# Kernel tuning notes

Measured on AMD Instinct MI355X. Metric: run time of the kernel, lower is better.

Reference implementation:

```python
import jax, jax.numpy as jnp
import numpy as np

EMPHASIS_FACTOR = 1.5
TOP_K_PERCENT = 0.2


def setup_inputs() -> dict:
    key = jax.random.key(0)
    k1, k2 = jax.random.split(key)
    B, S, D = 32, 8192, 256
    x = jax.random.normal(k1, (B, S, D), dtype=jnp.float32)
    W = jax.random.normal(k2, (D, 1), dtype=jnp.float32) * (1.0 / np.sqrt(D))
    b = jnp.zeros((1,), dtype=jnp.float32)
    return {"x": x, "W": W, "b": b}


def reference(x, W, b):
    B, S, D = x.shape
    # e = tanh(x @ W + b): [B, S, 1]
    e = jnp.tanh(jnp.einsum('bsd,do->bso', x, W) + b)
    # softmax over seq axis, squeeze -> [B, S]
    a = jax.nn.softmax(e, axis=1)[..., 0]
    # top-k selection: k = max(1, int(S * top_k_percent)), static under jit
    k = max(1, int(S * TOP_K_PERCENT))
    _, top_k_idx = jax.lax.top_k(a, k)  # [B, k]
    # mask of top-k positions (equiv to one_hot + reduce_max, but a direct scatter)
    mask = jnp.zeros((B, S), dtype=bool).at[jnp.arange(B)[:, None], top_k_idx].set(True)
    emphasized_a = jnp.where(mask, a * EMPHASIS_FACTOR, a)  # [B, S]
    # weighted sum over seq -> [B, D]
    summed_output = jnp.einsum('bsd,bs->bd', x, emphasized_a)
    return summed_output, emphasized_a
```

## Files before the change

kernel.cpp:

```cpp
#include <hip/hip_runtime.h>
#include <math.h>

#define BB 32
#define SS 8192
#define DD 256
#define K_SEL 1638
#define EMPH 1.5f
#define HBINS 2048
#define HCH 8
#define IDX_STRIDE 1664
#define K5_BLOCKS 8
#define K5_SLICE 205
#define NCHUNK 64
#define ROWS_PER_BLOCK (SS / NCHUNK)

__device__ __forceinline__ unsigned monokey(float f) {
    unsigned u = __float_as_uint(f);
    return u ^ ((u & 0x80000000u) ? 0xFFFFFFFFu : 0x80000000u);
}

__global__ __launch_bounds__(1024) void k1_e_hist_s1(const float* __restrict__ x,
                                                     const float* __restrict__ W,
                                                     const float* __restrict__ bias,
                                                     float* __restrict__ e_ws,
                                                     unsigned* __restrict__ hist_ws,
                                                     float* __restrict__ s1part,
                                                     float* __restrict__ zpart) {
    __shared__ unsigned hist[HBINS];
    __shared__ float red[16 * 256];
    __shared__ float zred;
    const int tid = threadIdx.x;
    const int lane = tid & 63;
    const int wv = tid >> 6;
    for (int i = tid; i < HBINS; i += 1024) hist[i] = 0;
    if (tid == 0) zred = 0.0f;

    const int b = blockIdx.x >> 3;
    const int ch = blockIdx.x & 7;
    const int row0 = ch * 1024;

    const float4* W4 = (const float4*)W;
    const int cg = lane & 15;
    const float4 w0 = W4[cg];
    const float4 w1 = W4[cg + 16];
    const float4 w2 = W4[cg + 32];
    const float4 w3 = W4[cg + 48];
    const float bias0 = bias[0];
    __syncthreads();

    const float* xb = x + (size_t)b * SS * DD;
    float* eb = e_ws + (size_t)b * SS;

    float acc[16];
    #pragma unroll
    for (int m = 0; m < 16; m++) acc[m] = 0.0f;
    float zloc = 0.0f;

    for (int it = 0; it < 16; it++) {
        const int r = row0 + (it * 16 + wv) * 4 + (lane >> 4);
        const float4* rp = (const float4*)(xb + (size_t)r * DD);
        float4 a0 = rp[cg];
        float4 a1 = rp[cg + 16];
        float4 a2 = rp[cg + 32];
        float4 a3 = rp[cg + 48];
        float p = a0.x * w0.x + a0.y * w0.y + a0.z * w0.z + a0.w * w0.w;
        p += a1.x * w1.x + a1.y * w1.y + a1.z * w1.z + a1.w * w1.w;
        p += a2.x * w2.x + a2.y * w2.y + a2.z * w2.z + a2.w * w2.w;
        p += a3.x * w3.x + a3.y * w3.y + a3.z * w3.z + a3.w * w3.w;
        p += __shfl_xor(p, 1, 64);
        p += __shfl_xor(p, 2, 64);
        p += __shfl_xor(p, 4, 64);
        p += __shfl_xor(p, 8, 64);
        float ev = tanhf(p + bias0);
        float w = expf(ev);
        if (cg == 0) {
            eb[r] = ev;
            atomicAdd(&hist[monokey(ev) >> 21], 1u);
            zloc += w;
        }
        acc[0] += w * a0.x;  acc[1] += w * a0.y;  acc[2] += w * a0.z;  acc[3] += w * a0.w;
        acc[4] += w * a1.x;  acc[5] += w * a1.y;  acc[6] += w * a1.z;  acc[7] += w * a1.w;
        acc[8] += w * a2.x;  acc[9] += w * a2.y;  acc[10] += w * a2.z; acc[11] += w * a2.w;
        acc[12] += w * a3.x; acc[13] += w * a3.y; acc[14] += w * a3.z; acc[15] += w * a3.w;
    }
    #pragma unroll
    for (int m = 0; m < 16; m++) {
        acc[m] += __shfl_xor(acc[m], 16, 64);
        acc[m] += __shfl_xor(acc[m], 32, 64);
    }
    zloc += __shfl_xor(zloc, 16, 64);
    zloc += __shfl_xor(zloc, 32, 64);
    if (lane == 0) atomicAdd(&zred, zloc);
    if (lane < 16) {
        #pragma unroll
        for (int m = 0; m < 16; m++) red[wv * 256 + lane * 16 + m] = acc[m];
    }
    __syncthreads();
    unsigned* hout = hist_ws + (size_t)blockIdx.x * HBINS;
    for (int i = tid; i < HBINS; i += 1024) hout[i] = hist[i];
    if (tid == 0) zpart[blockIdx.x] = zred;
    if (tid < 256) {
        const int d = tid;
        const int q = d >> 6;
        const int cg2 = (d >> 2) & 15;
        const int j = d & 3;
        const int m = q * 4 + j;
        float s = 0.0f;
        #pragma unroll
        for (int w = 0; w < 16; w++) s += red[w * 256 + cg2 * 16 + m];
        s1part[(size_t)blockIdx.x * DD + d] = s;
    }
}

__global__ __launch_bounds__(1024) void k2_select(const float* __restrict__ e_ws,
                                                  const unsigned* __restrict__ hist_ws,
                                                  const float* __restrict__ zpart,
                                                  float* __restrict__ ea_out,
                                                  float* __restrict__ zinv,
                                                  int* __restrict__ idx_ws) {
    const int b = blockIdx.x;
    const int tid = threadIdx.x;
    const int lane = tid & 63;
    const int wid = tid >> 6;

    __shared__ float se[SS];
    __shared__ unsigned binTot[HBINS];
    __shared__ unsigned gsuf[257];
    __shared__ unsigned hsuf[129];
    __shared__ unsigned h7[128];
    __shared__ unsigned ecnt[128];
    __shared__ unsigned ebase[128];
    __shared__ unsigned uvar[2];
    __shared__ unsigned selCnt;
    __shared__ float fvar;

    const float* eg = e_ws + (size_t)b * SS;
    float* og = ea_out + (size_t)b * SS;
    int* il = idx_ws + (size_t)b * IDX_STRIDE;

    #pragma unroll
    for (int i = 0; i < 8; i++) {
        int s = tid + i * 1024;
        se[s] = eg[s];
    }
    if (tid == 0) {
        float z = 0.0f;
        #pragma unroll
        for (int c = 0; c < HCH; c++) z += zpart[b * HCH + c];
        fvar = 1.0f / z;
        zinv[b] = fvar;
        selCnt = 0;
    }
    unsigned c0 = 0, c1 = 0;
    for (int ch = 0; ch < HCH; ch++) {
        const unsigned* hc = hist_ws + ((size_t)(b * HCH + ch)) * HBINS;
        c0 += hc[2 * tid];
        c1 += hc[2 * tid + 1];
    }
    binTot[2 * tid] = c0;
    binTot[2 * tid + 1] = c1;
    __syncthreads();

    if (wid == 0) {
        unsigned g[4];
        unsigned tot = 0;
        #pragma unroll
        for (int j = 0; j < 4; j++) {
            unsigned s = 0;
            #pragma unroll
            for (int m = 0; m < 8; m++) s += binTot[(lane * 4 + j) * 8 + m];
            g[j] = s;
            tot += s;
        }
        unsigned xx = tot;
        #pragma unroll
        for (int off = 1; off < 64; off <<= 1) {
            unsigned v = __shfl_down(xx, off, 64);
            if (lane + off < 64) xx += v;
        }
        unsigned Snext = __shfl_down(xx, 1, 64);
        if (lane == 63) Snext = 0;
        unsigned s3 = Snext + g[3];
        unsigned s2 = s3 + g[2];
        unsigned s1 = s2 + g[1];
        unsigned s0 = s1 + g[0];
        gsuf[4 * lane] = s0; gsuf[4 * lane + 1] = s1;
        gsuf[4 * lane + 2] = s2; gsuf[4 * lane + 3] = s3;
        if (lane == 63) gsuf[256] = 0;
    }
    __syncthreads();

    if (tid < 256) {
        unsigned above = gsuf[tid + 1];
        if (above < K_SEL && K_SEL <= gsuf[tid]) {
            unsigned running = above;
            for (int j = 7; j >= 0; j--) {
                unsigned c = binTot[tid * 8 + j];
                if (running < K_SEL && K_SEL <= running + c) {
                    uvar[0] = (unsigned)(tid * 8 + j);
                    uvar[1] = K_SEL - running;
                    break;
                }
                running += c;
            }
        }
    }
    __syncthreads();
    unsigned prefix = uvar[0];
    unsigned kk = uvar[1];

    #pragma unroll
    for (int pass = 0; pass < 3; pass++) {
        const int shift = 14 - 7 * pass;
        if (tid < 128) h7[tid] = 0;
        __syncthreads();
        #pragma unroll
        for (int i = 0; i < 8; i++) {
            unsigned key = monokey(se[tid + i * 1024]);
            if ((key >> (shift + 7)) == prefix)
                atomicAdd(&h7[(key >> shift) & 127u], 1u);
        }
        __syncthreads();
        if (wid == 0) {
            unsigned a0 = h7[2 * lane];
            unsigned a1 = h7[2 * lane + 1];
            unsigned tot = a0 + a1;
            unsigned xx = tot;
            #pragma unroll
            for (int off = 1; off < 64; off <<= 1) {
                unsigned v = __shfl_down(xx, off, 64);
                if (lane + off < 64) xx += v;
            }
            unsigned Snext = __shfl_down(xx, 1, 64);
            if (lane == 63) Snext = 0;
            unsigned t1 = Snext + a1;
            unsigned t0 = t1 + a0;
            hsuf[2 * lane] = t0;
            hsuf[2 * lane + 1] = t1;
            if (lane == 63) hsuf[128] = 0;
        }
        __syncthreads();
        if (tid < 128) {
            unsigned above = hsuf[tid + 1];
            if (above < kk && kk <= hsuf[tid]) {
                uvar[0] = (prefix << 7) | (unsigned)tid;
                uvar[1] = kk - above;
            }
        }
        __syncthreads();
        prefix = uvar[0];
        kk = uvar[1];
    }
    const unsigned T = prefix;
    const unsigned r = kk;
    const float invZ = fvar;

    #pragma unroll
    for (int c = 0; c < 8; c++) {
        int s = c * 1024 + tid;
        unsigned long long bal = __ballot(monokey(se[s]) == T);
        if (lane == 0) ecnt[c * 16 + wid] = (unsigned)__popcll(bal);
    }
    __syncthreads();
    if (wid == 0) {
        unsigned a0 = ecnt[2 * lane];
        unsigned a1 = ecnt[2 * lane + 1];
        unsigned tot = a0 + a1;
        unsigned xx = tot;
        #pragma unroll
        for (int off = 1; off < 64; off <<= 1) {
            unsigned v = __shfl_up(xx, off, 64);
            if (lane >= off) xx += v;
        }
        ebase[2 * lane] = xx - tot;
        ebase[2 * lane + 1] = xx - a1;
    }
    __syncthreads();
    #pragma unroll
    for (int c = 0; c < 8; c++) {
        int s = c * 1024 + tid;
        float v = se[s];
        unsigned key = monokey(v);
        bool eq = (key == T);
        bool gt = (key > T);
        unsigned long long bal = __ballot(eq);
        unsigned myPref = (unsigned)__popcll(bal & ((1ull << lane) - 1ull));
        unsigned rank = ebase[c * 16 + wid] + myPref;
        bool sel = gt || (eq && rank < r);
        float a = expf(v) * invZ;
        og[s] = sel ? a * EMPH : a;
        if (sel) {
            unsigned slot = atomicAdd(&selCnt, 1u);
            il[slot] = s;
        }
    }
}

__global__ __launch_bounds__(256) void k5_corr(const float* __restrict__ x,
                                               const float* __restrict__ ea,
                                               const int* __restrict__ idx_ws,
                                               float* __restrict__ corr) {
    const int b = blockIdx.x >> 3;
    const int j = blockIdx.x & 7;
    const int lane = threadIdx.x & 63;
    const int wid = threadIdx.x >> 6;
    const int lo = j * K5_SLICE;
    const int hi = (lo + K5_SLICE < K_SEL) ? lo + K5_SLICE : K_SEL;
    const int* il = idx_ws + (size_t)b * IDX_STRIDE;
    const float* xb = x + (size_t)b * SS * DD;
    const float* ab = ea + (size_t)b * SS;
    float4 acc = make_float4(0.f, 0.f, 0.f, 0.f);
    for (int t = lo + wid; t < hi; t += 4) {
        int s = il[t];
        float w = ab[s] * (1.0f / 3.0f);
        float4 x4 = ((const float4*)(xb + (size_t)s * DD))[lane];
        acc.x += w * x4.x; acc.y += w * x4.y; acc.z += w * x4.z; acc.w += w * x4.w;
    }
    __shared__ float lds[4 * 256];
    ((float4*)lds)[wid * 64 + lane] = acc;
    __syncthreads();
    const int t = threadIdx.x;
    float v = lds[t] + lds[256 + t] + lds[512 + t] + lds[768 + t];
    corr[(size_t)blockIdx.x * DD + t] = v;
}

__global__ __launch_bounds__(256) void k6_final(const float* __restrict__ s1part,
                                                const float* __restrict__ corr,
                                                const float* __restrict__ zinv,
                                                float* __restrict__ out) {
    const int b = blockIdx.x;
    const int d = threadIdx.x;
    float s1 = 0.0f;
    #pragma unroll
    for (int ch = 0; ch < HCH; ch++) s1 += s1part[((size_t)b * HCH + ch) * DD + d];
    float c = 0.0f;
    #pragma unroll
    for (int j = 0; j < K5_BLOCKS; j++) c += corr[((size_t)b * K5_BLOCKS + j) * DD + d];
    out[b * DD + d] = s1 * zinv[b] + c;
}

__global__ __launch_bounds__(256) void f1_dot_tanh(const float* __restrict__ x,
                                                   const float* __restrict__ W,
                                                   const float* __restrict__ bias,
                                                   float* __restrict__ e) {
    const int lane = threadIdx.x & 63;
    const int wib  = threadIdx.x >> 6;
    const int waveId = blockIdx.x * 4 + wib;
    const int totalWaves = gridDim.x * 4;
    const float4 w4 = ((const float4*)W)[lane];
    const float bias0 = bias[0];
    for (int row = waveId; row < BB * SS; row += totalWaves) {
        float4 x4 = ((const float4*)(x + (size_t)row * DD))[lane];
        float p = x4.x * w4.x + x4.y * w4.y + x4.z * w4.z + x4.w * w4.w;
        #pragma unroll
        for (int off = 32; off >= 1; off >>= 1)
            p += __shfl_xor(p, off, 64);
        if (lane == 0) e[row] = tanhf(p + bias0);
    }
}
__global__ __launch_bounds__(1024) void f2_softmax_topk(float* __restrict__ ea) {
    const int b = blockIdx.x;
    const int tid = threadIdx.x;
    const int lane = tid & 63;
    const int wid  = tid >> 6;
    __shared__ float se[SS];
    __shared__ float wredf[16];
    __shared__ unsigned hist[256];
    __shared__ unsigned ssum[256];
    __shared__ unsigned wcnt[16];
    __shared__ unsigned uvar[3];
    __shared__ float fvar[1];
    float* eg = ea + (size_t)b * SS;
    float lsum = 0.0f;
    #pragma unroll
    for (int i = 0; i < 8; i++) {
        int s = tid + i * 1024;
        float v = eg[s];
        se[s] = v;
        lsum += expf(v);
    }
    #pragma unroll
    for (int off = 32; off >= 1; off >>= 1)
        lsum += __shfl_xor(lsum, off, 64);
    if (lane == 0) wredf[wid] = lsum;
    __syncthreads();
    if (tid == 0) {
        float z = 0.0f;
        for (int w = 0; w < 16; w++) z += wredf[w];
        fvar[0] = 1.0f / z;
    }
    __syncthreads();
    const float invZ = fvar[0];
    unsigned kk = K_SEL;
    unsigned prefix = 0;
    for (int byte = 3; byte >= 0; byte--) {
        if (tid < 256) hist[tid] = 0;
        __syncthreads();
        #pragma unroll
        for (int i = 0; i < 8; i++) {
            unsigned key = monokey(se[tid + i * 1024]);
            bool active = (byte == 3) || ((key >> ((byte + 1) * 8)) == prefix);
            if (active) atomicAdd(&hist[(key >> (byte * 8)) & 0xFFu], 1u);
        }
        __syncthreads();
        if (tid < 256) ssum[tid] = hist[tid];
        __syncthreads();
        for (int off = 1; off < 256; off <<= 1) {
            unsigned add = 0;
            if (tid < 256 && tid + off < 256) add = ssum[tid + off];
            __syncthreads();
            if (tid < 256) ssum[tid] += add;
            __syncthreads();
        }
        if (tid < 256) {
            unsigned above = (tid == 255) ? 0u : ssum[tid + 1];
            if (above < kk && kk <= ssum[tid]) {
                uvar[0] = (unsigned)tid;
                uvar[1] = kk - above;
            }
        }
        __syncthreads();
        prefix = (prefix << 8) | uvar[0];
        kk = uvar[1];
        __syncthreads();
    }
    const unsigned T = prefix;
    const unsigned r = kk;
    if (tid == 0) uvar[2] = 0;
    __syncthreads();
    for (int chunk = 0; chunk < 8; chunk++) {
        int s = chunk * 1024 + tid;
        float v = se[s];
        unsigned key = monokey(v);
        bool gt = key > T;
        bool eq = (key == T);
        unsigned long long bal = __ballot(eq);
        unsigned waveTot = (unsigned)__popcll(bal);
        unsigned myPref = (unsigned)__popcll(bal & ((1ull << lane) - 1ull));
        if (lane == 0) wcnt[wid] = waveTot;
        __syncthreads();
        unsigned base = uvar[2];
        for (int w = 0; w < wid; w++) base += wcnt[w];
        bool sel = gt || (eq && (base + myPref) < r);
        float a = expf(v) * invZ;
        eg[s] = sel ? a * EMPH : a;
        __syncthreads();
        if (tid == 0) {
            unsigned t = uvar[2];
            for (int w = 0; w < 16; w++) t += wcnt[w];
            uvar[2] = t;
        }
        __syncthreads();
    }
}
__global__ __launch_bounds__(256) void f0_zero(float* __restrict__ p, int n) {
    int i = blockIdx.x * blockDim.x + threadIdx.x;
    if (i < n) p[i] = 0.0f;
}
__global__ __launch_bounds__(256) void f3_weighted_atomic(const float* __restrict__ x,
                                                          const float* __restrict__ ea,
                                                          float* __restrict__ out) {
    const int blk = blockIdx.x;
    const int b = blk / NCHUNK;
    const int chunk = blk % NCHUNK;
    const int lane = threadIdx.x & 63;
    const int wid  = threadIdx.x >> 6;
    const float* xb = x + ((size_t)b * SS + (size_t)chunk * ROWS_PER_BLOCK) * DD;
    const float* ab = ea + (size_t)b * SS + (size_t)chunk * ROWS_PER_BLOCK;
    float4 acc = make_float4(0.f, 0.f, 0.f, 0.f);
    for (int rr = wid; rr < ROWS_PER_BLOCK; rr += 4) {
        float4 x4 = ((const float4*)(xb + (size_t)rr * DD))[lane];
        float a = ab[rr];
        acc.x += x4.x * a; acc.y += x4.y * a; acc.z += x4.z * a; acc.w += x4.w * a;
    }
    __shared__ float lds[4 * 256];
    ((float4*)lds)[wid * 64 + lane] = acc;
    __syncthreads();
    const int t = threadIdx.x;
    float v = lds[t] + lds[256 + t] + lds[512 + t] + lds[768 + t];
    atomicAdd(&out[b * 256 + t], v);
}

extern "C" void kernel_launch(void* const* d_in, const int* in_sizes, int n_in,
                              void* d_out, int out_size, void* d_ws, size_t ws_size,
                              hipStream_t stream) {
    (void)in_sizes; (void)n_in; (void)out_size;
    const float* x    = (const float*)d_in[0];
    const float* W    = (const float*)d_in[1];
    const float* bias = (const float*)d_in[2];
    float* out = (float*)d_out;
    float* sum_out = out;
    float* ea = out + BB * DD;

    const size_t e_bytes    = (size_t)BB * SS * sizeof(float);
    const size_t hist_bytes = (size_t)BB * HCH * HBINS * sizeof(unsigned);
    const size_t s1_bytes   = (size_t)BB * HCH * DD * sizeof(float);
    const size_t corr_bytes = (size_t)BB * K5_BLOCKS * DD * sizeof(float);
    const size_t zinv_bytes = 128;
    const size_t zpart_bytes= (size_t)BB * HCH * sizeof(float);
    const size_t idx_bytes  = (size_t)BB * IDX_STRIDE * sizeof(int);
    const size_t need = e_bytes + hist_bytes + s1_bytes + corr_bytes + zinv_bytes
                      + zpart_bytes + idx_bytes;

    if (ws_size >= need) {
        char* p = (char*)d_ws;
        float*    e_ws    = (float*)p;                 p += e_bytes;
        unsigned* hist_ws = (unsigned*)p;              p += hist_bytes;
        float*    s1part  = (float*)p;                 p += s1_bytes;
        float*    corr    = (float*)p;                 p += corr_bytes;
        float*    zinv    = (float*)p;                 p += zinv_bytes;
        float*    zpart   = (float*)p;                 p += zpart_bytes;
        int*      idx_ws  = (int*)p;

        k1_e_hist_s1<<<BB * HCH, 1024, 0, stream>>>(x, W, bias, e_ws, hist_ws, s1part, zpart);
        k2_select<<<BB, 1024, 0, stream>>>(e_ws, hist_ws, zpart, ea, zinv, idx_ws);
        k5_corr<<<BB * K5_BLOCKS, 256, 0, stream>>>(x, ea, idx_ws, corr);
        k6_final<<<BB, 256, 0, stream>>>(s1part, corr, zinv, sum_out);
    } else {
        f1_dot_tanh<<<4096, 256, 0, stream>>>(x, W, bias, ea);
        f2_softmax_topk<<<BB, 1024, 0, stream>>>(ea);
        f0_zero<<<(BB * DD + 255) / 256, 256, 0, stream>>>(sum_out, BB * DD);
        f3_weighted_atomic<<<BB * NCHUNK, 256, 0, stream>>>(x, ea, sum_out);
    }
}
```

Measured before the change: 397.8 us.

## Split selection so output write and top-k correction run across 16 chunks per batch

The per-batch select kernel now only finds the threshold key and a per-chunk tie quota. A new kernel with 16 blocks per batch then writes the emphasized attention, gathers the selected indices into shared memory, and accumulates the correction sum directly, which removes the global index list and the 32-block serial write phase. The cost is per-iteration block syncs for the tie-rank bookkeeping and twice as many correction partials to reduce at the end.

```diff
diff --git a/kernel.cpp b/kernel.cpp
--- a/kernel.cpp
+++ b/kernel.cpp
@@ -8,9 +8,8 @@
 #define EMPH 1.5f
 #define HBINS 2048
 #define HCH 8
-#define IDX_STRIDE 1664
-#define K5_BLOCKS 8
-#define K5_SLICE 205
+#define NCH3 16
+#define CH3_ROWS (SS / NCH3)
 #define NCHUNK 64
 #define ROWS_PER_BLOCK (SS / NCHUNK)
 
@@ -112,12 +111,11 @@
     }
 }
 
-__global__ __launch_bounds__(1024) void k2_select(const float* __restrict__ e_ws,
+__global__ __launch_bounds__(1024) void k2_thresh(const float* __restrict__ e_ws,
                                                   const unsigned* __restrict__ hist_ws,
                                                   const float* __restrict__ zpart,
-                                                  float* __restrict__ ea_out,
                                                   float* __restrict__ zinv,
-                                                  int* __restrict__ idx_ws) {
+                                                  unsigned* __restrict__ tq_ws) {
     const int b = blockIdx.x;
     const int tid = threadIdx.x;
     const int lane = tid & 63;
@@ -128,15 +126,10 @@
     __shared__ unsigned gsuf[257];
     __shared__ unsigned hsuf[129];
     __shared__ unsigned h7[128];
-    __shared__ unsigned ecnt[128];
-    __shared__ unsigned ebase[128];
+    __shared__ unsigned tie16[NCH3];
     __shared__ unsigned uvar[2];
-    __shared__ unsigned selCnt;
-    __shared__ float fvar;
 
     const float* eg = e_ws + (size_t)b * SS;
-    float* og = ea_out + (size_t)b * SS;
-    int* il = idx_ws + (size_t)b * IDX_STRIDE;
 
     #pragma unroll
     for (int i = 0; i < 8; i++) {
@@ -147,9 +140,7 @@
         float z = 0.0f;
         #pragma unroll
         for (int c = 0; c < HCH; c++) z += zpart[b * HCH + c];
-        fvar = 1.0f / z;
-        zinv[b] = fvar;
-        selCnt = 0;
+        zinv[b] = 1.0f / z;
     }
     unsigned c0 = 0, c1 = 0;
     for (int ch = 0; ch < HCH; ch++) {
@@ -253,75 +244,112 @@
     }
     const unsigned T = prefix;
     const unsigned r = kk;
-    const float invZ = fvar;
-
-    #pragma unroll
-    for (int c = 0; c < 8; c++) {
-        int s = c * 1024 + tid;
-        unsigned long long bal = __ballot(monokey(se[s]) == T);
-        if (lane == 0) ecnt[c * 16 + wid] = (unsigned)__popcll(bal);
-    }
-    __syncthreads();
-    if (wid == 0) {
-        unsigned a0 = ecnt[2 * lane];
-        unsigned a1 = ecnt[2 * lane + 1];
-        unsigned tot = a0 + a1;
-        unsigned xx = tot;
-        #pragma unroll
-        for (int off = 1; off < 64; off <<= 1) {
-            unsigned v = __shfl_up(xx, off, 64);
-            if (lane >= off) xx += v;
-        }
-        ebase[2 * lane] = xx - tot;
-        ebase[2 * lane + 1] = xx - a1;
-    }
-    __syncthreads();
-    #pragma unroll
-    for (int c = 0; c < 8; c++) {
-        int s = c * 1024 + tid;
-        float v = se[s];
+
+    if (tid < NCH3) tie16[tid] = 0;
+    __syncthreads();
+    #pragma unroll
+    for (int i = 0; i < 8; i++) {
+        int s = i * 1024 + tid;
+        unsigned long long beq = __ballot(monokey(se[s]) == T);
+        if (lane == 0) atomicAdd(&tie16[s >> 9], (unsigned)__popcll(beq));
+    }
+    __syncthreads();
+    if (tid == 0) {
+        unsigned run = 0;
+        unsigned* tq = tq_ws + b * 32;
+        tq[0] = T;
+        for (int c = 0; c < NCH3; c++) {
+            unsigned tc = tie16[c];
+            unsigned q = (r > run) ? (r - run) : 0u;
+            if (q > tc) q = tc;
+            tq[1 + c] = q;
+            run += tc;
+        }
+    }
+}
+
+__global__ __launch_bounds__(256) void k3_write_corr(const float* __restrict__ x,
+                                                     const float* __restrict__ e_ws,
+                                                     const unsigned* __restrict__ tq_ws,
+                                                     const float* __restrict__ zinv,
+                                                     float* __restrict__ ea_out,
+                                                     float* __restrict__ corr) {
+    const int b = blockIdx.x >> 4;
+    const int ch = blockIdx.x & 15;
+    const int tid = threadIdx.x;
+    const int lane = tid & 63;
+    const int wid = tid >> 6;
+
+    const unsigned* tq = tq_ws + b * 32;
+    const unsigned T = tq[0];
+    const unsigned quota = tq[1 + ch];
+    const float invZ = zinv[b];
+    const int s0 = ch * CH3_ROWS;
+    const float* eg = e_ws + (size_t)b * SS;
+    float* og = ea_out + (size_t)b * SS;
+
+    __shared__ int lidx[CH3_ROWS];
+    __shared__ float lw[CH3_ROWS];
+    __shared__ float lds[4 * 256];
+    __shared__ unsigned wtie[4];
+    __shared__ unsigned tieRun;
+    __shared__ unsigned selCnt;
+    if (tid == 0) { tieRun = 0; selCnt = 0; }
+    __syncthreads();
+
+    #pragma unroll
+    for (int i = 0; i < CH3_ROWS / 256; i++) {
+        int s = s0 + i * 256 + tid;
+        float v = eg[s];
         unsigned key = monokey(v);
+        bool gt = key > T;
         bool eq = (key == T);
-        bool gt = (key > T);
-        unsigned long long bal = __ballot(eq);
-        unsigned myPref = (unsigned)__popcll(bal & ((1ull << lane) - 1ull));
-        unsigned rank = ebase[c * 16 + wid] + myPref;
-        bool sel = gt || (eq && rank < r);
+        unsigned long long beq = __ballot(eq);
+        if (lane == 0) wtie[wid] = (unsigned)__popcll(beq);
+        __syncthreads();
+        unsigned base = tieRun;
+        for (int w = 0; w < wid; w++) base += wtie[w];
+        unsigned rank = base + (unsigned)__popcll(beq & ((1ull << lane) - 1ull));
+        bool sel = gt || (eq && rank < quota);
         float a = expf(v) * invZ;
         og[s] = sel ? a * EMPH : a;
         if (sel) {
             unsigned slot = atomicAdd(&selCnt, 1u);
-            il[slot] = s;
-        }
-    }
-}
-
-__global__ __launch_bounds__(256) void k5_corr(const float* __restrict__ x,
-                                               const float* __restrict__ ea,
-                                               const int* __restrict__ idx_ws,
-                                               float* __restrict__ corr) {
-    const int b = blockIdx.x >> 3;
-    const int j = blockIdx.x & 7;
-    const int lane = threadIdx.x & 63;
-    const int wid = threadIdx.x >> 6;
-    const int lo = j * K5_SLICE;
-    const int hi = (lo + K5_SLICE < K_SEL) ? lo + K5_SLICE : K_SEL;
-    const int* il = idx_ws + (size_t)b * IDX_STRIDE;
+            lidx[slot] = s;
+            lw[slot] = 0.5f * a;
+        }
+        __syncthreads();
+        if (tid == 0) tieRun += wtie[0] + wtie[1] + wtie[2] + wtie[3];
+        __syncthreads();
+    }
+
     const float* xb = x + (size_t)b * SS * DD;
-    const float* ab = ea + (size_t)b * SS;
-    float4 acc = make_float4(0.f, 0.f, 0.f, 0.f);
-    for (int t = lo + wid; t < hi; t += 4) {
-        int s = il[t];
-        float w = ab[s] * (1.0f / 3.0f);
-        float4 x4 = ((const float4*)(xb + (size_t)s * DD))[lane];
-        acc.x += w * x4.x; acc.y += w * x4.y; acc.z += w * x4.z; acc.w += w * x4.w;
-    }
-    __shared__ float lds[4 * 256];
-    ((float4*)lds)[wid * 64 + lane] = acc;
-    __syncthreads();
-    const int t = threadIdx.x;
-    float v = lds[t] + lds[256 + t] + lds[512 + t] + lds[768 + t];
-    corr[(size_t)blockIdx.x * DD + t] = v;
+    const unsigned n = selCnt;
+    float4 acc0 = make_float4(0.f, 0.f, 0.f, 0.f);
+    float4 acc1 = make_float4(0.f, 0.f, 0.f, 0.f);
+    unsigned t = (unsigned)wid;
+    for (; t + 4 < n; t += 8) {
+        int sA = lidx[t];
+        int sB = lidx[t + 4];
+        float wA = lw[t];
+        float wB = lw[t + 4];
+        float4 a4 = ((const float4*)(xb + (size_t)sA * DD))[lane];
+        float4 b4 = ((const float4*)(xb + (size_t)sB * DD))[lane];
+        acc0.x += wA * a4.x; acc0.y += wA * a4.y; acc0.z += wA * a4.z; acc0.w += wA * a4.w;
+        acc1.x += wB * b4.x; acc1.y += wB * b4.y; acc1.z += wB * b4.z; acc1.w += wB * b4.w;
+    }
+    if (t < n) {
+        int sA = lidx[t];
+        float wA = lw[t];
+        float4 a4 = ((const float4*)(xb + (size_t)sA * DD))[lane];
+        acc0.x += wA * a4.x; acc0.y += wA * a4.y; acc0.z += wA * a4.z; acc0.w += wA * a4.w;
+    }
+    acc0.x += acc1.x; acc0.y += acc1.y; acc0.z += acc1.z; acc0.w += acc1.w;
+
+    ((float4*)lds)[wid * 64 + lane] = acc0;
+    __syncthreads();
+    float vv = lds[tid] + lds[256 + tid] + lds[512 + tid] + lds[768 + tid];
+    corr[(size_t)blockIdx.x * DD + tid] = vv;
 }
 
 __global__ __launch_bounds__(256) void k6_final(const float* __restrict__ s1part,
@@ -335,7 +363,7 @@
     for (int ch = 0; ch < HCH; ch++) s1 += s1part[((size_t)b * HCH + ch) * DD + d];
     float c = 0.0f;
     #pragma unroll
-    for (int j = 0; j < K5_BLOCKS; j++) c += corr[((size_t)b * K5_BLOCKS + j) * DD + d];
+    for (int j = 0; j < NCH3; j++) c += corr[((size_t)b * NCH3 + j) * DD + d];
     out[b * DD + d] = s1 * zinv[b] + c;
 }
 
@@ -495,12 +523,12 @@
     const size_t e_bytes    = (size_t)BB * SS * sizeof(float);
     const size_t hist_bytes = (size_t)BB * HCH * HBINS * sizeof(unsigned);
     const size_t s1_bytes   = (size_t)BB * HCH * DD * sizeof(float);
-    const size_t corr_bytes = (size_t)BB * K5_BLOCKS * DD * sizeof(float);
+    const size_t corr_bytes = (size_t)BB * NCH3 * DD * sizeof(float);
     const size_t zinv_bytes = 128;
     const size_t zpart_bytes= (size_t)BB * HCH * sizeof(float);
-    const size_t idx_bytes  = (size_t)BB * IDX_STRIDE * sizeof(int);
+    const size_t tq_bytes   = (size_t)BB * 32 * sizeof(unsigned);
     const size_t need = e_bytes + hist_bytes + s1_bytes + corr_bytes + zinv_bytes
-                      + zpart_bytes + idx_bytes;
+                      + zpart_bytes + tq_bytes;
 
     if (ws_size >= need) {
         char* p = (char*)d_ws;
@@ -510,11 +538,11 @@
         float*    corr    = (float*)p;                 p += corr_bytes;
         float*    zinv    = (float*)p;                 p += zinv_bytes;
         float*    zpart   = (float*)p;                 p += zpart_bytes;
-        int*      idx_ws  = (int*)p;
+        unsigned* tq_ws   = (unsigned*)p;
 
         k1_e_hist_s1<<<BB * HCH, 1024, 0, stream>>>(x, W, bias, e_ws, hist_ws, s1part, zpart);
-        k2_select<<<BB, 1024, 0, stream>>>(e_ws, hist_ws, zpart, ea, zinv, idx_ws);
-        k5_corr<<<BB * K5_BLOCKS, 256, 0, stream>>>(x, ea, idx_ws, corr);
+        k2_thresh<<<BB, 1024, 0, stream>>>(e_ws, hist_ws, zpart, zinv, tq_ws);
+        k3_write_corr<<<BB * NCH3, 256, 0, stream>>>(x, e_ws, tq_ws, zinv, ea, corr);
         k6_final<<<BB, 256, 0, stream>>>(s1part, corr, zinv, sum_out);
     } else {
         f1_dot_tanh<<<4096, 256, 0, stream>>>(x, W, bias, ea);
```

New measurement: 380.5 us. 1.05x faster.
